# Kernel tuning notes

Hardware: AMD Instinct MI355X
Metric: run time of the kernel (lower is better)

## Reference

```python
import jax, jax.numpy as jnp
import numpy as np

N = 20000          # nodes
F = 256            # num_node_features (== num_sampled_vectors)
FEAT_EMB = 63      # feat_emb_dim
EMB = FEAT_EMB + 1 # emb_dim = feat_emb_dim + val_emb_dim
CH = F * EMB       # 16384, conv1 input channels
HID = 128
OUT = 7
E = 320000         # edges


def setup_inputs() -> dict:
    key = jax.random.key(0)
    ks = jax.random.split(key, 7)
    x = jax.random.normal(ks[0], (N, F), dtype=jnp.float32)
    emb_table = jax.random.normal(ks[1], (F, FEAT_EMB), dtype=jnp.float32) * 0.02
    W1 = jax.random.normal(ks[2], (CH, HID), dtype=jnp.float32) / np.sqrt(CH)
    b1 = jnp.zeros((HID,), jnp.float32)
    W2 = jax.random.normal(ks[3], (HID, OUT), dtype=jnp.float32) / np.sqrt(HID)
    b2 = jnp.zeros((OUT,), jnp.float32)
    edge_index = jax.random.randint(ks[4], (2, E), 0, N, dtype=jnp.int32)
    return {"x": x, "emb_table": emb_table, "W1": W1, "b1": b1,
            "W2": W2, "b2": b2, "edge_index": edge_index}


def _gcn_conv(h, W, b, src, dst, norm, n):
    # PyG GCNConv: symmetric-normalized aggregation (with self loops) of x @ W, then + bias
    h = h @ W                                   # [n, out]
    msg = h[src] * norm[:, None]                # gather + edge-weight
    agg = jax.ops.segment_sum(msg, dst, num_segments=n)  # scatter-add
    return agg + b


def reference(x, emb_table, W1, b1, W2, b2, edge_index):
    n = x.shape[0]
    # StandardScaler: per-feature zero mean, unit (population) std
    mean = x.mean(axis=0)
    std = x.std(axis=0)
    std = jnp.where(std == 0, jnp.float32(1.0), std)
    xs = (x - mean) / std                       # [n, F]
    # feature embedding construction: per node, concat emb_table with its value column
    feats = jnp.concatenate(
        [jnp.broadcast_to(emb_table[None], (n, F, FEAT_EMB)), xs[:, :, None]],
        axis=-1,
    ).reshape(n, CH)                            # [n, F*EMB]
    # GCN normalization with self loops (eval mode: no dropout_adj / dropout)
    loop = jnp.arange(n, dtype=edge_index.dtype)
    src = jnp.concatenate([edge_index[0], loop])
    dst = jnp.concatenate([edge_index[1], loop])
    deg = jax.ops.segment_sum(jnp.ones_like(src, jnp.float32), dst, num_segments=n)
    dinv = jnp.where(deg > 0, jax.lax.rsqrt(deg), jnp.float32(0.0))
    norm = dinv[src] * dinv[dst]                # [E+n]
    h = jax.nn.relu(_gcn_conv(feats, W1, b1, src, dst, norm, n))
    out = _gcn_conv(h, W2, b2, src, dst, norm, n)
    return jax.nn.log_softmax(out, axis=1)
```

## Files before the change

### kernel.cpp

```cpp
#include <hip/hip_runtime.h>
#include <math.h>

#define F_   256
#define FEAT_EMB_ 63
#define HID_ 128
#define OUT_ 7
#define SLOTS 64
#define NP 16

typedef short short8 __attribute__((ext_vector_type(8)));
typedef float f32x4 __attribute__((ext_vector_type(4)));

__device__ inline short f2bf(float f) {
    unsigned u = __float_as_uint(f);
    u += 0x7FFFu + ((u >> 16) & 1u);
    return (short)(u >> 16);
}

#define K1_CS 625
#define K1_ED 625
#define K1_CV 256
#define K1_PK 16
#define K1_GRID (K1_CS + K1_ED + K1_CV + K1_PK)

__global__ __launch_bounds__(256) void k1_kernel(const float* __restrict__ x,
                                                 const int* __restrict__ ei,
                                                 const float* __restrict__ emb,
                                                 const float* __restrict__ W1,
                                                 float* __restrict__ colsum16,
                                                 float* __restrict__ colsq16,
                                                 int* __restrict__ deg,
                                                 int* __restrict__ adjP,
                                                 float* __restrict__ Cp16,
                                                 short* __restrict__ Wfrag, int E) {
    __shared__ float4 smem[8 * 64];
    int b = blockIdx.x;
    int t = threadIdx.x;

    if (b < K1_CS) {
        int rl = t >> 6, lane = t & 63;
        int row0 = b * 32 + rl * 8;
        float4 v[8];
#pragma unroll
        for (int i = 0; i < 8; i++)
            v[i] = *(const float4*)(x + (size_t)(row0 + i) * F_ + lane * 4);
        float4 s = make_float4(0.f, 0.f, 0.f, 0.f);
        float4 q = make_float4(0.f, 0.f, 0.f, 0.f);
#pragma unroll
        for (int i = 0; i < 8; i++) {
            s.x += v[i].x; s.y += v[i].y; s.z += v[i].z; s.w += v[i].w;
            q.x += v[i].x * v[i].x; q.y += v[i].y * v[i].y;
            q.z += v[i].z * v[i].z; q.w += v[i].w * v[i].w;
        }
        smem[rl * 64 + lane] = s;
        smem[(rl + 4) * 64 + lane] = q;
        __syncthreads();
        if (rl == 0) {
#pragma unroll
            for (int i = 1; i < 4; i++) {
                float4 a = smem[i * 64 + lane], bq = smem[(i + 4) * 64 + lane];
                s.x += a.x; s.y += a.y; s.z += a.z; s.w += a.w;
                q.x += bq.x; q.y += bq.y; q.z += bq.z; q.w += bq.w;
            }
            int buf = (b & (NP - 1)) * F_;
            atomicAdd(&colsum16[buf + lane * 4 + 0], s.x);
            atomicAdd(&colsum16[buf + lane * 4 + 1], s.y);
            atomicAdd(&colsum16[buf + lane * 4 + 2], s.z);
            atomicAdd(&colsum16[buf + lane * 4 + 3], s.w);
            atomicAdd(&colsq16[buf + lane * 4 + 0], q.x);
            atomicAdd(&colsq16[buf + lane * 4 + 1], q.y);
            atomicAdd(&colsq16[buf + lane * 4 + 2], q.z);
            atomicAdd(&colsq16[buf + lane * 4 + 3], q.w);
        }
    } else if (b < K1_CS + K1_ED) {
        int e0 = (b - K1_CS) * 512 + t;
#pragma unroll
        for (int i = 0; i < 2; i++) {
            int e = e0 + i * 256;
            if (e < E) {
                int s = ei[e];
                int d = ei[E + e];
                int pos = atomicAdd(&deg[d], 1);
                if (pos < SLOTS) adjP[(d << 6) + pos] = s;
            }
        }
    } else if (b < K1_CS + K1_ED + K1_CV) {
        int f = b - (K1_CS + K1_ED);
        int jg = t >> 5, k4 = t & 31;
        float4 s = make_float4(0.f, 0.f, 0.f, 0.f);
        for (int j = jg; j < FEAT_EMB_; j += 8) {
            float e = emb[f * FEAT_EMB_ + j];
            float4 w = *(const float4*)(W1 + ((size_t)(f * 64 + j)) * HID_ + k4 * 4);
            s.x += e * w.x; s.y += e * w.y; s.z += e * w.z; s.w += e * w.w;
        }
        smem[jg * 32 + k4] = s;
        __syncthreads();
        if (jg == 0) {
#pragma unroll
            for (int i = 1; i < 8; i++) {
                float4 a = smem[i * 32 + k4];
                s.x += a.x; s.y += a.y; s.z += a.z; s.w += a.w;
            }
            int buf = (f & (NP - 1)) * HID_;
            atomicAdd(&Cp16[buf + k4 * 4 + 0], s.x);
            atomicAdd(&Cp16[buf + k4 * 4 + 1], s.y);
            atomicAdd(&Cp16[buf + k4 * 4 + 2], s.z);
            atomicAdd(&Cp16[buf + k4 * 4 + 3], s.w);
        }
    } else {
        int pb = b - (K1_CS + K1_ED + K1_CV);
        int f0 = pb * 16;
#pragma unroll
        for (int i = 0; i < 8; i++) {
            int idx = t + i * 256;
            int f = f0 + (idx >> 7);
            int nn = idx & 127;
            float w = W1[((size_t)(f * 64 + 63)) * HID_ + nn];
            int kc = f >> 5, j = f & 7, hi2 = (f >> 3) & 3;
            int lane = hi2 * 16 + (nn & 15);
            int nt = nn >> 4;
            Wfrag[(((kc * 8 + nt) * 64 + lane) << 3) + j] = f2bf(w);
        }
    }
}

__global__ __launch_bounds__(256) void mm1_kernel(const float* __restrict__ x,
                                                  const short* __restrict__ Wfrag,
                                                  const float* __restrict__ Cp16,
                                                  const float* __restrict__ colsum16,
                                                  const float* __restrict__ colsq16,
                                                  const int* __restrict__ deg,
                                                  unsigned short* __restrict__ g0b,
                                                  int n) {
    __shared__ float cps[HID_];
    __shared__ float smean[F_];
    __shared__ float srstd[F_];
    int t = threadIdx.x;
    {
        float s = 0.f, q = 0.f;
#pragma unroll
        for (int p = 0; p < NP; p++) {
            s += colsum16[p * F_ + t];
            q += colsq16[p * F_ + t];
        }
        float m = s / (float)n;
        float var = fmaxf(q / (float)n - m * m, 0.f);
        float sd = sqrtf(var);
        smean[t] = m;
        srstd[t] = (sd == 0.f) ? 1.f : (1.f / sd);
    }
    if (t < HID_) {
        float s = 0.f;
#pragma unroll
        for (int p = 0; p < NP; p++) s += Cp16[p * HID_ + t];
        cps[t] = s;
    }
    __syncthreads();

    int wave = t >> 6, lane = t & 63;
    int m = lane & 15;
    int hi = lane >> 4;
    int rowbase = blockIdx.x * 64 + wave * 16;
    int arow = rowbase + m;
    bool rok = arow < n;
    const float* xrow = x + (size_t)arow * F_ + hi * 8;

    float4 xa[8], xb[8];
    if (rok) {
#pragma unroll
        for (int kc = 0; kc < 8; kc++) {
            xa[kc] = *(const float4*)(xrow + kc * 32);
            xb[kc] = *(const float4*)(xrow + kc * 32 + 4);
        }
    }

    const float4* smv = (const float4*)smean;
    const float4* srv = (const float4*)srstd;

    f32x4 acc[8];
#pragma unroll
    for (int i = 0; i < 8; i++) acc[i] = (f32x4){0.f, 0.f, 0.f, 0.f};

#pragma unroll
    for (int kc = 0; kc < 8; kc++) {
        short8 af;
        if (rok) {
            int mb = kc * 8 + hi * 2;
            float4 m0 = smv[mb], m1 = smv[mb + 1];
            float4 r0 = srv[mb], r1 = srv[mb + 1];
            af[0] = f2bf((xa[kc].x - m0.x) * r0.x);
            af[1] = f2bf((xa[kc].y - m0.y) * r0.y);
            af[2] = f2bf((xa[kc].z - m0.z) * r0.z);
            af[3] = f2bf((xa[kc].w - m0.w) * r0.w);
            af[4] = f2bf((xb[kc].x - m1.x) * r1.x);
            af[5] = f2bf((xb[kc].y - m1.y) * r1.y);
            af[6] = f2bf((xb[kc].z - m1.z) * r1.z);
            af[7] = f2bf((xb[kc].w - m1.w) * r1.w);
        } else {
            af = (short8){0, 0, 0, 0, 0, 0, 0, 0};
        }
#pragma unroll
        for (int nt = 0; nt < 8; nt++) {
            short8 bf = *(const short8*)(Wfrag + (((kc * 8 + nt) * 64 + lane) << 3));
            acc[nt] = __builtin_amdgcn_mfma_f32_16x16x32_bf16(af, bf, acc[nt], 0, 0, 0);
        }
    }

    float dv[4];
#pragma unroll
    for (int r = 0; r < 4; r++) {
        int gr = rowbase + hi * 4 + r;
        dv[r] = (gr < n) ? rsqrtf((float)deg[gr] + 1.0f) : 0.f;
    }
#pragma unroll
    for (int nt = 0; nt < 8; nt++) {
        int col = nt * 16 + m;
        float cp = cps[col];
#pragma unroll
        for (int r = 0; r < 4; r++) {
            int gr = rowbase + hi * 4 + r;
            if (gr < n)
                g0b[(size_t)gr * HID_ + col] = (unsigned short)f2bf((acc[nt][r] + cp) * dv[r]);
        }
    }
}

__global__ __launch_bounds__(256) void agg_fc2_kernel(const unsigned short* __restrict__ g0b,
                                                      const int* __restrict__ deg,
                                                      const int* __restrict__ adjP,
                                                      const float* __restrict__ b1,
                                                      const float* __restrict__ W2,
                                                      float* __restrict__ g2, int n) {
    int wave = threadIdx.x >> 6;
    int lane = threadIdx.x & 63;
    int d = blockIdx.x * 4 + wave;
    if (d >= n) return;

    int dgv = deg[d];
    int o0 = d << 6;
    int o1 = o0 + min(dgv, SLOTS);
    unsigned u = *(const unsigned*)(g0b + (size_t)d * HID_ + lane * 2);
    float ax = __uint_as_float(u << 16);
    float ay = __uint_as_float(u & 0xFFFF0000u);

    for (int base = o0; base < o1; base += 64) {
        int idx = (base + lane < o1) ? adjP[base + lane] : 0;
        int c2 = min(64, o1 - base);
        int j = 0;
        for (; j + 4 <= c2; j += 4) {
            int s0 = __shfl(idx, j + 0);
            int s1 = __shfl(idx, j + 1);
            int s2 = __shfl(idx, j + 2);
            int s3 = __shfl(idx, j + 3);
            unsigned u0 = *(const unsigned*)(g0b + (size_t)s0 * HID_ + lane * 2);
            unsigned u1 = *(const unsigned*)(g0b + (size_t)s1 * HID_ + lane * 2);
            unsigned u2 = *(const unsigned*)(g0b + (size_t)s2 * HID_ + lane * 2);
            unsigned u3 = *(const unsigned*)(g0b + (size_t)s3 * HID_ + lane * 2);
            ax += __uint_as_float(u0 << 16) + __uint_as_float(u1 << 16)
                + __uint_as_float(u2 << 16) + __uint_as_float(u3 << 16);
            ay += __uint_as_float(u0 & 0xFFFF0000u) + __uint_as_float(u1 & 0xFFFF0000u)
                + __uint_as_float(u2 & 0xFFFF0000u) + __uint_as_float(u3 & 0xFFFF0000u);
        }
        for (; j < c2; j++) {
            int s = __shfl(idx, j);
            unsigned uu = *(const unsigned*)(g0b + (size_t)s * HID_ + lane * 2);
            ax += __uint_as_float(uu << 16);
            ay += __uint_as_float(uu & 0xFFFF0000u);
        }
    }

    float dv = rsqrtf((float)dgv + 1.0f);
    float2 bb = *(const float2*)(b1 + lane * 2);
    float h0 = fmaxf(ax * dv + bb.x, 0.f);
    float h1 = fmaxf(ay * dv + bb.y, 0.f);

    const float* w2a = W2 + (lane * 2) * OUT_;
    const float* w2b = W2 + (lane * 2 + 1) * OUT_;
    float r[OUT_];
#pragma unroll
    for (int c = 0; c < OUT_; c++) {
        float p = h0 * w2a[c] + h1 * w2b[c];
#pragma unroll
        for (int off = 32; off > 0; off >>= 1) p += __shfl_xor(p, off);
        r[c] = p;
    }
    if (lane < 8) {
        float val;
        switch (lane) {
            case 0: val = r[0]; break;
            case 1: val = r[1]; break;
            case 2: val = r[2]; break;
            case 3: val = r[3]; break;
            case 4: val = r[4]; break;
            case 5: val = r[5]; break;
            case 6: val = r[6]; break;
            default: val = 0.f; break;
        }
        g2[(size_t)d * 8 + lane] = val * dv;
    }
}

__global__ __launch_bounds__(256) void agg2_softmax_kernel(const float* __restrict__ g2,
                                                           const int* __restrict__ deg,
                                                           const int* __restrict__ adjP,
                                                           const float* __restrict__ b2,
                                                           float* __restrict__ out, int n) {
    int t = threadIdx.x;
    int g = t >> 3;
    int c = t & 7;
    int d = blockIdx.x * 32 + g;
    if (d >= n) return;

    int dgv = deg[d];
    int o0 = d << 6;
    int o1 = o0 + min(dgv, SLOTS);
    float acc = g2[(size_t)d * 8 + c];
    int i = o0;
    for (; i + 2 <= o1; i += 2) {
        int s0 = adjP[i], s1 = adjP[i + 1];
        acc += g2[(size_t)s0 * 8 + c] + g2[(size_t)s1 * 8 + c];
    }
    for (; i < o1; i++) acc += g2[(size_t)adjP[i] * 8 + c];

    float dv = rsqrtf((float)dgv + 1.0f);
    float z = (c < OUT_) ? (acc * dv + b2[c]) : -INFINITY;
    float m = z;
#pragma unroll
    for (int off = 4; off > 0; off >>= 1) m = fmaxf(m, __shfl_xor(m, off, 8));
    float e = (c < OUT_) ? __expf(z - m) : 0.f;
    float sum = e;
#pragma unroll
    for (int off = 4; off > 0; off >>= 1) sum += __shfl_xor(sum, off, 8);
    if (c < OUT_) out[(size_t)d * OUT_ + c] = z - m - __logf(sum);
}

extern "C" void kernel_launch(void* const* d_in, const int* in_sizes, int n_in,
                              void* d_out, int out_size, void* d_ws, size_t ws_size,
                              hipStream_t stream) {
    const float* x    = (const float*)d_in[0];
    const float* emb  = (const float*)d_in[1];
    const float* W1   = (const float*)d_in[2];
    const float* b1   = (const float*)d_in[3];
    const float* W2   = (const float*)d_in[4];
    const float* b2   = (const float*)d_in[5];
    const int*   ei   = (const int*)d_in[6];
    float* out = (float*)d_out;

    const int N = in_sizes[0] / F_;
    const int E = in_sizes[6] / 2;

    float* ws = (float*)d_ws;
    size_t o = 0;
    float* colsum16 = ws + o; o += NP * F_;
    float* colsq16  = ws + o; o += NP * F_;
    float* Cp16     = ws + o; o += NP * HID_;
    int*   deg      = (int*)(ws + o); o += N;
    size_t zero_elems = o;
    short* Wfrag    = (short*)(ws + o); o += (size_t)F_ * HID_ / 2;
    int*   adjP     = (int*)(ws + o); o += (size_t)N * SLOTS;
    unsigned short* g0b = (unsigned short*)(ws + o); o += (size_t)N * HID_ / 2;
    float* g2       = ws + o; o += (size_t)N * 8;

    hipMemsetAsync(ws, 0, zero_elems * sizeof(float), stream);
    k1_kernel<<<K1_GRID, 256, 0, stream>>>(x, ei, emb, W1, colsum16, colsq16,
                                           deg, adjP, Cp16, Wfrag, E);
    mm1_kernel<<<(N + 63) / 64, 256, 0, stream>>>(x, Wfrag, Cp16, colsum16, colsq16,
                                                  deg, g0b, N);
    agg_fc2_kernel<<<(N + 3) / 4, 256, 0, stream>>>(g0b, deg, adjP, b1, W2, g2, N);
    agg2_softmax_kernel<<<(N + 31) / 32, 256, 0, stream>>>(g2, deg, adjP, b2, out, N);
}
```

Measured before the change: 147.7 us.

## Fold standardization into W1 and feed mm1 a bf16 copy of x

The per-feature mean and inverse std are folded into the value-column weights and a bias-correction vector in a new small k2 kernel, so mm1 no longer computes column statistics or normalizes each row. k1 also writes a bf16 copy of x, which mm1 reads at half the bandwidth. The cost is an extra kernel launch, an extra bf16 write of x, and applying bf16 rounding to raw x instead of to standardized x, which could lose precision when means are large.

```diff
diff --git a/kernel.cpp b/kernel.cpp
--- a/kernel.cpp
+++ b/kernel.cpp
@@ -20,8 +20,7 @@
 #define K1_CS 625
 #define K1_ED 625
 #define K1_CV 256
-#define K1_PK 16
-#define K1_GRID (K1_CS + K1_ED + K1_CV + K1_PK)
+#define K1_GRID (K1_CS + K1_ED + K1_CV)
 
 __global__ __launch_bounds__(256) void k1_kernel(const float* __restrict__ x,
                                                  const int* __restrict__ ei,
@@ -32,7 +31,8 @@
                                                  int* __restrict__ deg,
                                                  int* __restrict__ adjP,
                                                  float* __restrict__ Cp16,
-                                                 short* __restrict__ Wfrag, int E) {
+                                                 unsigned short* __restrict__ xb,
+                                                 int E) {
     __shared__ float4 smem[8 * 64];
     int b = blockIdx.x;
     int t = threadIdx.x;
@@ -44,6 +44,15 @@
 #pragma unroll
         for (int i = 0; i < 8; i++)
             v[i] = *(const float4*)(x + (size_t)(row0 + i) * F_ + lane * 4);
+#pragma unroll
+        for (int i = 0; i < 8; i++) {
+            ushort4 o;
+            o.x = (unsigned short)f2bf(v[i].x);
+            o.y = (unsigned short)f2bf(v[i].y);
+            o.z = (unsigned short)f2bf(v[i].z);
+            o.w = (unsigned short)f2bf(v[i].w);
+            *(ushort4*)(xb + (size_t)(row0 + i) * F_ + lane * 4) = o;
+        }
         float4 s = make_float4(0.f, 0.f, 0.f, 0.f);
         float4 q = make_float4(0.f, 0.f, 0.f, 0.f);
 #pragma unroll
@@ -84,7 +93,7 @@
                 if (pos < SLOTS) adjP[(d << 6) + pos] = s;
             }
         }
-    } else if (b < K1_CS + K1_ED + K1_CV) {
+    } else {
         int f = b - (K1_CS + K1_ED);
         int jg = t >> 5, k4 = t & 31;
         float4 s = make_float4(0.f, 0.f, 0.f, 0.f);
@@ -107,54 +116,71 @@
             atomicAdd(&Cp16[buf + k4 * 4 + 2], s.z);
             atomicAdd(&Cp16[buf + k4 * 4 + 3], s.w);
         }
-    } else {
-        int pb = b - (K1_CS + K1_ED + K1_CV);
-        int f0 = pb * 16;
-#pragma unroll
-        for (int i = 0; i < 8; i++) {
-            int idx = t + i * 256;
-            int f = f0 + (idx >> 7);
-            int nn = idx & 127;
-            float w = W1[((size_t)(f * 64 + 63)) * HID_ + nn];
-            int kc = f >> 5, j = f & 7, hi2 = (f >> 3) & 3;
-            int lane = hi2 * 16 + (nn & 15);
-            int nt = nn >> 4;
-            Wfrag[(((kc * 8 + nt) * 64 + lane) << 3) + j] = f2bf(w);
-        }
-    }
-}
-
-__global__ __launch_bounds__(256) void mm1_kernel(const float* __restrict__ x,
+    }
+}
+
+__global__ __launch_bounds__(256) void k2_kernel(const float* __restrict__ W1,
+                                                 const float* __restrict__ colsum16,
+                                                 const float* __restrict__ colsq16,
+                                                 const float* __restrict__ Cp16,
+                                                 short* __restrict__ Wfrag,
+                                                 float* __restrict__ CpF, int n) {
+    __shared__ float sm[32], sr[32];
+    __shared__ float red[256];
+    int b = blockIdx.x;
+    int t = threadIdx.x;
+    if (t < 32) {
+        int f = b * 32 + t;
+        float s = 0.f, q = 0.f;
+#pragma unroll
+        for (int p = 0; p < NP; p++) {
+            s += colsum16[p * F_ + f];
+            q += colsq16[p * F_ + f];
+        }
+        float m = s / (float)n;
+        float var = fmaxf(q / (float)n - m * m, 0.f);
+        float sd = sqrtf(var);
+        sm[t] = m;
+        sr[t] = (sd == 0.f) ? 1.f : (1.f / sd);
+    }
+    __syncthreads();
+    int nn = t & 127, fs = t >> 7;
+    float cacc = 0.f;
+#pragma unroll
+    for (int i = 0; i < 16; i++) {
+        int fl = i * 2 + fs;
+        int f = b * 32 + fl;
+        float w = W1[((size_t)(f * 64 + 63)) * HID_ + nn];
+        float wr = w * sr[fl];
+        cacc -= sm[fl] * wr;
+        int kc = f >> 5, j = f & 7, hi2 = (f >> 3) & 3;
+        int lane = hi2 * 16 + (nn & 15);
+        int nt = nn >> 4;
+        Wfrag[(((kc * 8 + nt) * 64 + lane) << 3) + j] = f2bf(wr);
+    }
+    red[t] = cacc;
+    __syncthreads();
+    if (t < 128) {
+        float v = red[t] + red[t + 128];
+        if (b == 0) {
+            float s = 0.f;
+#pragma unroll
+            for (int p = 0; p < NP; p++) s += Cp16[p * HID_ + t];
+            v += s;
+        }
+        atomicAdd(&CpF[t], v);
+    }
+}
+
+__global__ __launch_bounds__(256) void mm1_kernel(const unsigned short* __restrict__ xb,
                                                   const short* __restrict__ Wfrag,
-                                                  const float* __restrict__ Cp16,
-                                                  const float* __restrict__ colsum16,
-                                                  const float* __restrict__ colsq16,
+                                                  const float* __restrict__ CpF,
                                                   const int* __restrict__ deg,
                                                   unsigned short* __restrict__ g0b,
                                                   int n) {
     __shared__ float cps[HID_];
-    __shared__ float smean[F_];
-    __shared__ float srstd[F_];
     int t = threadIdx.x;
-    {
-        float s = 0.f, q = 0.f;
-#pragma unroll
-        for (int p = 0; p < NP; p++) {
-            s += colsum16[p * F_ + t];
-            q += colsq16[p * F_ + t];
-        }
-        float m = s / (float)n;
-        float var = fmaxf(q / (float)n - m * m, 0.f);
-        float sd = sqrtf(var);
-        smean[t] = m;
-        srstd[t] = (sd == 0.f) ? 1.f : (1.f / sd);
-    }
-    if (t < HID_) {
-        float s = 0.f;
-#pragma unroll
-        for (int p = 0; p < NP; p++) s += Cp16[p * HID_ + t];
-        cps[t] = s;
-    }
+    if (t < HID_) cps[t] = CpF[t];
     __syncthreads();
 
     int wave = t >> 6, lane = t & 63;
@@ -163,19 +189,18 @@
     int rowbase = blockIdx.x * 64 + wave * 16;
     int arow = rowbase + m;
     bool rok = arow < n;
-    const float* xrow = x + (size_t)arow * F_ + hi * 8;
-
-    float4 xa[8], xb[8];
+    const unsigned short* xrow = xb + (size_t)arow * F_ + hi * 8;
+
+    short8 af[8];
     if (rok) {
 #pragma unroll
-        for (int kc = 0; kc < 8; kc++) {
-            xa[kc] = *(const float4*)(xrow + kc * 32);
-            xb[kc] = *(const float4*)(xrow + kc * 32 + 4);
-        }
-    }
-
-    const float4* smv = (const float4*)smean;
-    const float4* srv = (const float4*)srstd;
+        for (int kc = 0; kc < 8; kc++)
+            af[kc] = *(const short8*)(xrow + kc * 32);
+    } else {
+#pragma unroll
+        for (int kc = 0; kc < 8; kc++)
+            af[kc] = (short8){0, 0, 0, 0, 0, 0, 0, 0};
+    }
 
     f32x4 acc[8];
 #pragma unroll
@@ -183,26 +208,10 @@
 
 #pragma unroll
     for (int kc = 0; kc < 8; kc++) {
-        short8 af;
-        if (rok) {
-            int mb = kc * 8 + hi * 2;
-            float4 m0 = smv[mb], m1 = smv[mb + 1];
-            float4 r0 = srv[mb], r1 = srv[mb + 1];
-            af[0] = f2bf((xa[kc].x - m0.x) * r0.x);
-            af[1] = f2bf((xa[kc].y - m0.y) * r0.y);
-            af[2] = f2bf((xa[kc].z - m0.z) * r0.z);
-            af[3] = f2bf((xa[kc].w - m0.w) * r0.w);
-            af[4] = f2bf((xb[kc].x - m1.x) * r1.x);
-            af[5] = f2bf((xb[kc].y - m1.y) * r1.y);
-            af[6] = f2bf((xb[kc].z - m1.z) * r1.z);
-            af[7] = f2bf((xb[kc].w - m1.w) * r1.w);
-        } else {
-            af = (short8){0, 0, 0, 0, 0, 0, 0, 0};
-        }
 #pragma unroll
         for (int nt = 0; nt < 8; nt++) {
             short8 bf = *(const short8*)(Wfrag + (((kc * 8 + nt) * 64 + lane) << 3));
-            acc[nt] = __builtin_amdgcn_mfma_f32_16x16x32_bf16(af, bf, acc[nt], 0, 0, 0);
+            acc[nt] = __builtin_amdgcn_mfma_f32_16x16x32_bf16(af[kc], bf, acc[nt], 0, 0, 0);
         }
     }
 
@@ -354,18 +363,20 @@
     float* colsum16 = ws + o; o += NP * F_;
     float* colsq16  = ws + o; o += NP * F_;
     float* Cp16     = ws + o; o += NP * HID_;
+    float* CpF      = ws + o; o += HID_;
     int*   deg      = (int*)(ws + o); o += N;
     size_t zero_elems = o;
     short* Wfrag    = (short*)(ws + o); o += (size_t)F_ * HID_ / 2;
+    unsigned short* xb = (unsigned short*)(ws + o); o += (size_t)N * F_ / 2;
     int*   adjP     = (int*)(ws + o); o += (size_t)N * SLOTS;
     unsigned short* g0b = (unsigned short*)(ws + o); o += (size_t)N * HID_ / 2;
     float* g2       = ws + o; o += (size_t)N * 8;
 
     hipMemsetAsync(ws, 0, zero_elems * sizeof(float), stream);
     k1_kernel<<<K1_GRID, 256, 0, stream>>>(x, ei, emb, W1, colsum16, colsq16,
-                                           deg, adjP, Cp16, Wfrag, E);
-    mm1_kernel<<<(N + 63) / 64, 256, 0, stream>>>(x, Wfrag, Cp16, colsum16, colsq16,
-                                                  deg, g0b, N);
+                                           deg, adjP, Cp16, xb, E);
+    k2_kernel<<<8, 256, 0, stream>>>(W1, colsum16, colsq16, Cp16, Wfrag, CpF, N);
+    mm1_kernel<<<(N + 63) / 64, 256, 0, stream>>>(xb, Wfrag, CpF, deg, g0b, N);
     agg_fc2_kernel<<<(N + 3) / 4, 256, 0, stream>>>(g0b, deg, adjP, b1, W2, g2, N);
     agg2_softmax_kernel<<<(N + 31) / 32, 256, 0, stream>>>(g2, deg, adjP, b2, out, N);
 }
```

New measurement: 148.7 us. About the same (+0.7%).
